# Kernel tuning notes

Hardware: AMD Instinct MI355X
Metric: run time of the kernel (lower is better)

Reference implementation:

```python
import jax, jax.numpy as jnp
import numpy as np

N_NODES = 50000
N_EDGES = 800000
D = 128
L = 3


def setup_inputs() -> dict:
    key = jax.random.key(0)
    ks = jax.random.split(key, 16)
    x = jax.random.normal(ks[0], (N_NODES, D), dtype=jnp.float32)
    edge_index = jax.random.randint(ks[1], (2, N_EDGES), 0, N_NODES, dtype=jnp.int32)
    # ensure every node has at least one incoming edge (degree > 0)
    edge_index = edge_index.at[1, :N_NODES].set(jnp.arange(N_NODES, dtype=jnp.int32))
    edge_attr = jax.random.normal(ks[2], (N_EDGES, 1), dtype=jnp.float32)
    s = 1.0 / np.sqrt(D)
    lin_w = jax.random.normal(ks[3], (L, 1, D), dtype=jnp.float32)          # edge_dim=1 -> D
    lin_b = jax.random.normal(ks[4], (L, D), dtype=jnp.float32) * s
    eps = jnp.zeros((L,), dtype=jnp.float32)                                 # initial_eps = 0, trainable
    w1 = jax.random.normal(ks[5], (L, D, D), dtype=jnp.float32) * s
    b1 = jax.random.normal(ks[6], (L, D), dtype=jnp.float32) * s
    w2 = jax.random.normal(ks[7], (L, D, D), dtype=jnp.float32) * s
    b2 = jax.random.normal(ks[8], (L, D), dtype=jnp.float32) * s
    d_cat = D + L * D
    final_w = jax.random.normal(ks[9], (d_cat, D), dtype=jnp.float32) / np.sqrt(d_cat)
    final_b = jax.random.normal(ks[10], (D,), dtype=jnp.float32) * s
    return {"x": x, "edge_index": edge_index, "edge_attr": edge_attr,
            "lin_w": lin_w, "lin_b": lin_b, "eps": eps,
            "w1": w1, "b1": b1, "w2": w2, "b2": b2,
            "final_w": final_w, "final_b": final_b}


def reference(x, edge_index, edge_attr, lin_w, lin_b, eps, w1, b1, w2, b2, final_w, final_b):
    src, tgt = edge_index[0], edge_index[1]
    n = x.shape[0]
    # degree of target nodes (float), shape [N, 1]
    deg = jax.ops.segment_sum(jnp.ones(src.shape[0], x.dtype), tgt, num_segments=n)[:, None]
    xs = [x]
    h = x
    for l in range(L):
        e = edge_attr @ lin_w[l] + lin_b[l]                  # [E, D] edge-feature projection
        msg = jax.nn.relu(h[src] + e)                        # gather + fuse + relu
        agg = jax.ops.segment_sum(msg, tgt, num_segments=n)  # scatter-add
        out = agg / deg + (1.0 + eps[l]) * h                 # degree-normalize + eps-residual
        h = jax.nn.relu(out @ w1[l] + b1[l]) @ w2[l] + b2[l] # 2-layer MLP (no BN, no dropout)
        xs.append(h)
    cat = jnp.concatenate(xs, axis=-1)                       # [N, D + L*D]
    return cat @ final_w + final_b
```

## Files before the change

kernel.cpp:

```cpp
#include <hip/hip_runtime.h>

#define NN 50000
#define NE 800000
#define DIM 128
#define NLAYERS 3

typedef __attribute__((ext_vector_type(8))) short bf16x8;
typedef __attribute__((ext_vector_type(4))) float f32x4;

__device__ __forceinline__ unsigned short f2bf_hi(float f) {
    unsigned int u = __float_as_uint(f);
    u += 0x7FFF + ((u >> 16) & 1);
    return (unsigned short)(u >> 16);
}
__device__ __forceinline__ float bf2f(unsigned short u) {
    return __uint_as_float(((unsigned int)u) << 16);
}

__global__ __launch_bounds__(256) void rank_kernel(const int* __restrict__ tgt,
                                                   int* __restrict__ counts,
                                                   int* __restrict__ rank, int E) {
    int base = (blockIdx.x * 256 + threadIdx.x) * 4;
    if (base >= E) return;
    int4 t = *(const int4*)(tgt + base);
    int4 r;
    r.x = atomicAdd(&counts[t.x], 1);
    r.y = atomicAdd(&counts[t.y], 1);
    r.z = atomicAdd(&counts[t.z], 1);
    r.w = atomicAdd(&counts[t.w], 1);
    *(int4*)(rank + base) = r;
}

__global__ __launch_bounds__(256) void scan_partial_kernel(const int* __restrict__ counts,
                                                           int* __restrict__ psum, int n) {
    __shared__ int ws[4];
    int b = blockIdx.x, t = threadIdx.x;
    int idx = b * 1024 + t * 4;
    int v = 0;
    if (idx < n) {
        int4 c = *(const int4*)(counts + idx);
        v = c.x + c.y + c.z + c.w;
    }
#pragma unroll
    for (int o = 32; o > 0; o >>= 1) v += __shfl_xor(v, o);
    int lane = t & 63, wid = t >> 6;
    if (lane == 0) ws[wid] = v;
    __syncthreads();
    if (t == 0) psum[b] = ws[0] + ws[1] + ws[2] + ws[3];
}

__global__ __launch_bounds__(64) void scan_small_kernel(const int* __restrict__ psum,
                                                        int* __restrict__ pbase,
                                                        int* __restrict__ offsets,
                                                        int nb, int n) {
    int lane = threadIdx.x;
    int v = (lane < nb) ? psum[lane] : 0;
    int incl = v;
#pragma unroll
    for (int o = 1; o < 64; o <<= 1) {
        int t = __shfl_up(incl, o);
        if (lane >= o) incl += t;
    }
    if (lane < nb) pbase[lane] = incl - v;
    if (lane == 63) offsets[n] = incl;
}

__global__ __launch_bounds__(256) void scan_apply_kernel(const int* __restrict__ counts,
                                                         const int* __restrict__ pbase,
                                                         int* __restrict__ offsets, int n) {
    __shared__ int ws[4];
    int b = blockIdx.x, t = threadIdx.x;
    int lane = t & 63, wid = t >> 6;
    int idx = b * 1024 + t * 4;
    int4 c = make_int4(0, 0, 0, 0);
    if (idx < n) c = *(const int4*)(counts + idx);
    int tsum = c.x + c.y + c.z + c.w;
    int incl = tsum;
#pragma unroll
    for (int o = 1; o < 64; o <<= 1) {
        int tt = __shfl_up(incl, o);
        if (lane >= o) incl += tt;
    }
    if (lane == 63) ws[wid] = incl;
    __syncthreads();
    int wbase = pbase[b];
    for (int w = 0; w < wid; w++) wbase += ws[w];
    if (idx < n) {
        int e0 = wbase + incl - tsum;
        int4 o;
        o.x = e0;
        o.y = e0 + c.x;
        o.z = o.y + c.y;
        o.w = o.z + c.z;
        *(int4*)(offsets + idx) = o;
    }
}

__global__ __launch_bounds__(256) void scatter2_kernel(
    const int* __restrict__ src, const int* __restrict__ tgt,
    const float* __restrict__ ea, const int* __restrict__ rank,
    const int* __restrict__ offsets, int2* __restrict__ sedge, int E) {
    int base = (blockIdx.x * 256 + threadIdx.x) * 4;
    if (base >= E) return;
    int4 s = *(const int4*)(src + base);
    int4 t = *(const int4*)(tgt + base);
    int4 r = *(const int4*)(rank + base);
    float4 a = *(const float4*)(ea + base);
    sedge[offsets[t.x] + r.x] = make_int2(s.x << 8, __float_as_int(a.x));
    sedge[offsets[t.y] + r.y] = make_int2(s.y << 8, __float_as_int(a.y));
    sedge[offsets[t.z] + r.z] = make_int2(s.z << 8, __float_as_int(a.z));
    sedge[offsets[t.w] + r.w] = make_int2(s.w << 8, __float_as_int(a.w));
}

__device__ __forceinline__ int packidx(int k, int c) {
    return (((k >> 5) << 3) + (c >> 4)) * 512 + (((k >> 3) & 3) << 7) + ((c & 15) << 3) + (k & 7);
}

#define XCVT_T 1600000

__global__ __launch_bounds__(256) void prep_kernel(
    const float* __restrict__ x, unsigned short* __restrict__ xb,
    const float* __restrict__ w1, const float* __restrict__ w2, const float* __restrict__ fw,
    unsigned short* __restrict__ w1t_h, unsigned short* __restrict__ w1t_l,
    unsigned short* __restrict__ w2t_h, unsigned short* __restrict__ w2t_l,
    unsigned short* __restrict__ fwt_h, unsigned short* __restrict__ fwt_l) {
    int gid = blockIdx.x * 256 + threadIdx.x;
    if (gid < XCVT_T) {
        int i = gid * 4;
        float4 v = *(const float4*)(x + i);
        ushort4 o;
        o.x = f2bf_hi(v.x); o.y = f2bf_hi(v.y);
        o.z = f2bf_hi(v.z); o.w = f2bf_hi(v.w);
        *(ushort4*)(xb + i) = o;
        return;
    }
    int g0 = gid - XCVT_T;
    float v; int oidx;
    unsigned short *oh, *ol;
    if (g0 < 49152) {
        int l = g0 >> 14, rem = g0 & 16383, k = rem >> 7, c = rem & 127;
        v = w1[g0]; oidx = l * 16384 + packidx(k, c); oh = w1t_h; ol = w1t_l;
    } else if (g0 < 98304) {
        int g = g0 - 49152;
        int l = g >> 14, rem = g & 16383, k = rem >> 7, c = rem & 127;
        v = w2[g]; oidx = l * 16384 + packidx(k, c); oh = w2t_h; ol = w2t_l;
    } else if (g0 < 163840) {
        int g = g0 - 98304;
        int k = g >> 7, c = g & 127;
        v = fw[g]; oidx = packidx(k, c); oh = fwt_h; ol = fwt_l;
    } else return;
    unsigned short h = f2bf_hi(v);
    float lo = v - bf2f(h);
    oh[oidx] = h;
    ol[oidx] = f2bf_hi(lo);
}

__global__ __launch_bounds__(256, 8) void agg_kernel(
    const unsigned short* __restrict__ hprev, const int* __restrict__ offs,
    const int2* __restrict__ sedge,
    const float* __restrict__ lw, const float* __restrict__ lb,
    const float* __restrict__ epsp, int layer,
    unsigned short* __restrict__ aggh, unsigned short* __restrict__ aggl, int N) {
    int g = threadIdx.x >> 4;
    int r = threadIdx.x & 15;
    int node = blockIdx.x * 16 + g;
    if (node >= N) return;
    int d0 = r * 8;
    float lwv[8], lbv[8];
    *(float4*)&lwv[0] = *(const float4*)(lw + d0);
    *(float4*)&lwv[4] = *(const float4*)(lw + d0 + 4);
    *(float4*)&lbv[0] = *(const float4*)(lb + d0);
    *(float4*)&lbv[4] = *(const float4*)(lb + d0 + 4);
    const char* hb = (const char*)hprev + r * 16;

    int s0 = offs[node], s1 = offs[node + 1];
    int sm = s1 - 1;
    int cnt = s1 - s0;
    float a[8];
#pragma unroll
    for (int c = 0; c < 8; c++) a[c] = 0.f;

    int2 e0 = sedge[s0];
    int2 e1 = sedge[min(s0 + 1, sm)];
    int2 e2 = sedge[min(s0 + 2, sm)];
    int2 e3 = sedge[min(s0 + 3, sm)];
    uint4 h0 = *(const uint4*)(hb + (unsigned)e0.x);
    uint4 h1 = *(const uint4*)(hb + (unsigned)e1.x);
    uint4 h2 = *(const uint4*)(hb + (unsigned)e2.x);

    for (int it = s0; it < s1; ++it) {
        uint4 h3 = *(const uint4*)(hb + (unsigned)e3.x);
        int2 e4 = sedge[min(it + 4, sm)];
        float wgt = __int_as_float(e0.y);
        unsigned uu[4] = {h0.x, h0.y, h0.z, h0.w};
#pragma unroll
        for (int c = 0; c < 4; c++) {
            float f0 = __uint_as_float(uu[c] << 16);
            float f1 = __uint_as_float(uu[c] & 0xffff0000u);
            a[2 * c]     += fmaxf(f0 + fmaf(wgt, lwv[2 * c], lbv[2 * c]), 0.f);
            a[2 * c + 1] += fmaxf(f1 + fmaf(wgt, lwv[2 * c + 1], lbv[2 * c + 1]), 0.f);
        }
        e0 = e1; e1 = e2; e2 = e3; e3 = e4;
        h0 = h1; h1 = h2; h2 = h3;
    }

    float inv = 1.f / (float)cnt;
    float ge = 1.f + epsp[layer];
    uint4 hs = *(const uint4*)(hb + ((unsigned)node << 8));
    unsigned su[4] = {hs.x, hs.y, hs.z, hs.w};
    unsigned short hh[8], hl[8];
#pragma unroll
    for (int c = 0; c < 4; c++) {
        float f0 = __uint_as_float(su[c] << 16);
        float f1 = __uint_as_float(su[c] & 0xffff0000u);
        float v0 = a[2 * c] * inv + ge * f0;
        float v1 = a[2 * c + 1] * inv + ge * f1;
        unsigned short h0v = f2bf_hi(v0), h1v = f2bf_hi(v1);
        hh[2 * c] = h0v; hh[2 * c + 1] = h1v;
        hl[2 * c] = f2bf_hi(v0 - bf2f(h0v));
        hl[2 * c + 1] = f2bf_hi(v1 - bf2f(h1v));
    }
    unsigned short* ph = aggh + (size_t)node * DIM + d0;
    unsigned short* pl = aggl + (size_t)node * DIM + d0;
    *(ushort4*)ph       = *(const ushort4*)&hh[0];
    *(ushort4*)(ph + 4) = *(const ushort4*)&hh[4];
    *(ushort4*)pl       = *(const ushort4*)&hl[0];
    *(ushort4*)(pl + 4) = *(const ushort4*)&hl[4];
}

#define HSTR 136

#define MLP1_LOAD(T, Bh_, Bl_, Ah_, Al_) do {                               \
    int k0_ = (T) * 32;                                                     \
    _Pragma("unroll")                                                       \
    for (int j_ = 0; j_ < 2; j_++) {                                        \
        size_t ro_ = (size_t)rowc[j_] * DIM + k0_ + q * 8;                  \
        Bh_[j_] = *(const bf16x8*)(ah_g + ro_);                             \
        Bl_[j_] = *(const bf16x8*)(al_g + ro_);                             \
    }                                                                       \
    _Pragma("unroll")                                                       \
    for (int i_ = 0; i_ < 4; i_++) {                                        \
        size_t co_ = ((size_t)((T) * 8 + wr * 4 + i_) << 9) + lane * 8;     \
        Ah_[i_] = *(const bf16x8*)(w1h + co_);                              \
        Al_[i_] = *(const bf16x8*)(w1l + co_);                              \
    }                                                                       \
} while (0)

#define MLP2_LOADW(T, Ah_, Al_) do {                                        \
    _Pragma("unroll")                                                       \
    for (int i_ = 0; i_ < 4; i_++) {                                        \
        size_t co_ = ((size_t)((T) * 8 + wr * 4 + i_) << 9) + lane * 8;     \
        Ah_[i_] = *(const bf16x8*)(w2h + co_);                              \
        Al_[i_] = *(const bf16x8*)(w2l + co_);                              \
    }                                                                       \
} while (0)

#define MLP2_LOADB(T, Bh_, Bl_) do {                                        \
    int k0_ = (T) * 32;                                                     \
    _Pragma("unroll")                                                       \
    for (int j_ = 0; j_ < 2; j_++) {                                        \
        int so_ = (wc * 32 + j_ * 16 + lr) * HSTR + k0_ + q * 8;            \
        Bh_[j_] = *(const bf16x8*)&s_hh[so_];                               \
        Bl_[j_] = *(const bf16x8*)&s_hl[so_];                               \
    }                                                                       \
} while (0)

#define MLP_MFMA(Bh_, Bl_, Ah_, Al_) do {                                   \
    _Pragma("unroll")                                                       \
    for (int i_ = 0; i_ < 4; i_++)                                          \
        _Pragma("unroll")                                                   \
        for (int j_ = 0; j_ < 2; j_++) {                                    \
            acc[i_][j_] = __builtin_amdgcn_mfma_f32_16x16x32_bf16(Ah_[i_], Bh_[j_], acc[i_][j_], 0, 0, 0); \
            acc[i_][j_] = __builtin_amdgcn_mfma_f32_16x16x32_bf16(Ah_[i_], Bl_[j_], acc[i_][j_], 0, 0, 0); \
            acc[i_][j_] = __builtin_amdgcn_mfma_f32_16x16x32_bf16(Al_[i_], Bh_[j_], acc[i_][j_], 0, 0, 0); \
        }                                                                   \
} while (0)

#define MLP_PHASES_12()                                                     \
    f32x4 acc[4][2];                                                        \
    _Pragma("unroll")                                                       \
    for (int i = 0; i < 4; i++)                                             \
        _Pragma("unroll")                                                   \
        for (int j = 0; j < 2; j++) acc[i][j] = (f32x4)(0.f);               \
    bf16x8 pBh[2], pBl[2], pAh[4], pAl[4];                                  \
    bf16x8 qBh[2], qBl[2], qAh[4], qAl[4];                                  \
    MLP1_LOAD(0, pBh, pBl, pAh, pAl);                                       \
    MLP1_LOAD(1, qBh, qBl, qAh, qAl);                                       \
    MLP_MFMA(pBh, pBl, pAh, pAl);                                           \
    MLP1_LOAD(2, pBh, pBl, pAh, pAl);                                       \
    MLP_MFMA(qBh, qBl, qAh, qAl);                                           \
    MLP1_LOAD(3, qBh, qBl, qAh, qAl);                                       \
    MLP_MFMA(pBh, pBl, pAh, pAl);                                           \
    MLP_MFMA(qBh, qBl, qAh, qAl);                                           \
    MLP2_LOADW(0, pAh, pAl);                                                \
    _Pragma("unroll")                                                       \
    for (int i = 0; i < 4; i++) {                                           \
        int hc0 = wr * 64 + i * 16 + q * 4;                                 \
        float4 bv = *(const float4*)(b1 + hc0);                             \
        float bvr[4] = {bv.x, bv.y, bv.z, bv.w};                            \
        _Pragma("unroll")                                                   \
        for (int j = 0; j < 2; j++) {                                       \
            int nl = wc * 32 + j * 16 + lr;                                 \
            unsigned short hh[4], hl[4];                                    \
            _Pragma("unroll")                                               \
            for (int r = 0; r < 4; r++) {                                   \
                float v = fmaxf(acc[i][j][r] + bvr[r], 0.f);                \
                unsigned short h = f2bf_hi(v);                              \
                hh[r] = h;                                                  \
                hl[r] = f2bf_hi(v - bf2f(h));                               \
            }                                                               \
            *(ushort4*)&s_hh[nl * HSTR + hc0] = *(const ushort4*)&hh[0];    \
            *(ushort4*)&s_hl[nl * HSTR + hc0] = *(const ushort4*)&hl[0];    \
        }                                                                   \
    }                                                                       \
    __syncthreads();                                                        \
    _Pragma("unroll")                                                       \
    for (int i = 0; i < 4; i++)                                             \
        _Pragma("unroll")                                                   \
        for (int j = 0; j < 2; j++) acc[i][j] = (f32x4)(0.f);               \
    MLP2_LOADB(0, pBh, pBl);                                                \
    MLP2_LOADW(1, qAh, qAl);                                                \
    MLP2_LOADB(1, qBh, qBl);                                                \
    MLP_MFMA(pBh, pBl, pAh, pAl);                                           \
    MLP2_LOADW(2, pAh, pAl);                                                \
    MLP2_LOADB(2, pBh, pBl);                                                \
    MLP_MFMA(qBh, qBl, qAh, qAl);                                           \
    MLP2_LOADW(3, qAh, qAl);                                                \
    MLP2_LOADB(3, qBh, qBl);                                                \
    MLP_MFMA(pBh, pBl, pAh, pAl);                                           \
    MLP_MFMA(qBh, qBl, qAh, qAl);

__global__ __launch_bounds__(256, 3) void mlp_fused(
    const unsigned short* __restrict__ ah_g, const unsigned short* __restrict__ al_g,
    const unsigned short* __restrict__ w1h, const unsigned short* __restrict__ w1l,
    const float* __restrict__ b1,
    const unsigned short* __restrict__ w2h, const unsigned short* __restrict__ w2l,
    const float* __restrict__ b2,
    unsigned short* __restrict__ out, int N) {
    __shared__ unsigned short s_hh[64 * HSTR], s_hl[64 * HSTR];
    int tid = threadIdx.x;
    int lane = tid & 63, w = tid >> 6;
    int q = lane >> 4, lr = lane & 15;
    int wr = w >> 1, wc = w & 1;
    int n0 = blockIdx.x * 64;
    int nb0 = n0 + wc * 32 + lr;
    int rowc[2];
    rowc[0] = min(nb0, N - 1);
    rowc[1] = min(nb0 + 16, N - 1);

    MLP_PHASES_12();

#pragma unroll
    for (int i = 0; i < 4; i++) {
        int hc0 = wr * 64 + i * 16 + q * 4;
        float4 bv = *(const float4*)(b2 + hc0);
        float bvr[4] = {bv.x, bv.y, bv.z, bv.w};
#pragma unroll
        for (int j = 0; j < 2; j++) {
            int node = nb0 + j * 16;
            if (node < N) {
                unsigned short o[4];
#pragma unroll
                for (int r = 0; r < 4; r++) o[r] = f2bf_hi(acc[i][j][r] + bvr[r]);
                *(ushort4*)&out[(size_t)node * DIM + hc0] = *(const ushort4*)&o[0];
            }
        }
    }
}

#define FIN3_LOADG(T, Bv_, Ah_, Al_) do {                                   \
    const unsigned short* asrc_ = srcs3[(T) >> 2];                          \
    int kk_ = ((T) & 3) * 32;                                               \
    _Pragma("unroll")                                                       \
    for (int j_ = 0; j_ < 2; j_++) {                                        \
        size_t ro_ = (size_t)rowc[j_] * DIM + kk_ + q * 8;                  \
        Bv_[j_] = *(const bf16x8*)(asrc_ + ro_);                            \
    }                                                                       \
    _Pragma("unroll")                                                       \
    for (int i_ = 0; i_ < 4; i_++) {                                        \
        size_t co_ = ((size_t)((T) * 8 + wr * 4 + i_) << 9) + lane * 8;     \
        Ah_[i_] = *(const bf16x8*)(fwh + co_);                              \
        Al_[i_] = *(const bf16x8*)(fwl + co_);                              \
    }                                                                       \
} while (0)

#define FIN_MFMA(Bv_, Ah_, Al_) do {                                        \
    _Pragma("unroll")                                                       \
    for (int i_ = 0; i_ < 4; i_++)                                          \
        _Pragma("unroll")                                                   \
        for (int j_ = 0; j_ < 2; j_++) {                                    \
            acc[i_][j_] = __builtin_amdgcn_mfma_f32_16x16x32_bf16(Ah_[i_], Bv_[j_], acc[i_][j_], 0, 0, 0); \
            acc[i_][j_] = __builtin_amdgcn_mfma_f32_16x16x32_bf16(Al_[i_], Bv_[j_], acc[i_][j_], 0, 0, 0); \
        }                                                                   \
} while (0)

#define FIN3_STEPL(T) do {                                                  \
    int kk_ = ((T) - 12) * 32;                                              \
    bf16x8 Bh_[2], Bl_[2], Ah_[4], Al_[4];                                  \
    _Pragma("unroll")                                                       \
    for (int j_ = 0; j_ < 2; j_++) {                                        \
        int so_ = (wc * 32 + j_ * 16 + lr) * HSTR + kk_ + q * 8;            \
        Bh_[j_] = *(const bf16x8*)&s_hh[so_];                               \
        Bl_[j_] = *(const bf16x8*)&s_hl[so_];                               \
    }                                                                       \
    _Pragma("unroll")                                                       \
    for (int i_ = 0; i_ < 4; i_++) {                                        \
        size_t co_ = ((size_t)((T) * 8 + wr * 4 + i_) << 9) + lane * 8;     \
        Ah_[i_] = *(const bf16x8*)(fwh + co_);                              \
        Al_[i_] = *(const bf16x8*)(fwl + co_);                              \
    }                                                                       \
    _Pragma("unroll")                                                       \
    for (int i_ = 0; i_ < 4; i_++)                                          \
        _Pragma("unroll")                                                   \
        for (int j_ = 0; j_ < 2; j_++) {                                    \
            acc[i_][j_] = __builtin_amdgcn_mfma_f32_16x16x32_bf16(Ah_[i_], Bh_[j_], acc[i_][j_], 0, 0, 0); \
            acc[i_][j_] = __builtin_amdgcn_mfma_f32_16x16x32_bf16(Ah_[i_], Bl_[j_], acc[i_][j_], 0, 0, 0); \
            acc[i_][j_] = __builtin_amdgcn_mfma_f32_16x16x32_bf16(Al_[i_], Bh_[j_], acc[i_][j_], 0, 0, 0); \
        }                                                                   \
} while (0)

__global__ __launch_bounds__(256, 3) void mlp_final_fused(
    const unsigned short* __restrict__ ah_g, const unsigned short* __restrict__ al_g,
    const unsigned short* __restrict__ w1h, const unsigned short* __restrict__ w1l,
    const float* __restrict__ b1,
    const unsigned short* __restrict__ w2h, const unsigned short* __restrict__ w2l,
    const float* __restrict__ b2,
    const unsigned short* __restrict__ xsrc, const unsigned short* __restrict__ h0p,
    const unsigned short* __restrict__ h1p,
    const unsigned short* __restrict__ fwh, const unsigned short* __restrict__ fwl,
    const float* __restrict__ fbias, float* __restrict__ out, int N) {
    __shared__ unsigned short s_hh[64 * HSTR], s_hl[64 * HSTR];
    int tid = threadIdx.x;
    int lane = tid & 63, w = tid >> 6;
    int q = lane >> 4, lr = lane & 15;
    int wr = w >> 1, wc = w & 1;
    int n0 = blockIdx.x * 64;
    int nb0 = n0 + wc * 32 + lr;
    int rowc[2];
    rowc[0] = min(nb0, N - 1);
    rowc[1] = min(nb0 + 16, N - 1);

    MLP_PHASES_12();

    __syncthreads();

#pragma unroll
    for (int i = 0; i < 4; i++) {
        int hc0 = wr * 64 + i * 16 + q * 4;
        float4 bv = *(const float4*)(b2 + hc0);
        float bvr[4] = {bv.x, bv.y, bv.z, bv.w};
#pragma unroll
        for (int j = 0; j < 2; j++) {
            int nl = wc * 32 + j * 16 + lr;
            unsigned short hh[4], hl[4];
#pragma unroll
            for (int r = 0; r < 4; r++) {
                float v = acc[i][j][r] + bvr[r];
                unsigned short h = f2bf_hi(v);
                hh[r] = h;
                hl[r] = f2bf_hi(v - bf2f(h));
            }
            *(ushort4*)&s_hh[nl * HSTR + hc0] = *(const ushort4*)&hh[0];
            *(ushort4*)&s_hl[nl * HSTR + hc0] = *(const ushort4*)&hl[0];
        }
    }

#pragma unroll
    for (int i = 0; i < 4; i++)
#pragma unroll
        for (int j = 0; j < 2; j++) acc[i][j] = (f32x4)(0.f);

    const unsigned short* srcs3[3] = {xsrc, h0p, h1p};
    bf16x8 pB[2], pWh[4], pWl[4];
    bf16x8 qB[2], qWh[4], qWl[4];
    FIN3_LOADG(0, pB, pWh, pWl);
    FIN3_LOADG(1, qB, qWh, qWl);
    __syncthreads();

#pragma unroll
    for (int t = 0; t < 12; t += 2) {
        FIN_MFMA(pB, pWh, pWl);
        if (t + 2 < 12) FIN3_LOADG(t + 2, pB, pWh, pWl);
        FIN_MFMA(qB, qWh, qWl);
        if (t + 3 < 12) FIN3_LOADG(t + 3, qB, qWh, qWl);
    }
    FIN3_STEPL(12);
    FIN3_STEPL(13);
    FIN3_STEPL(14);
    FIN3_STEPL(15);

#pragma unroll
    for (int i = 0; i < 4; i++) {
        int hc0 = wr * 64 + i * 16 + q * 4;
        float4 bv = *(const float4*)(fbias + hc0);
        float bvr[4] = {bv.x, bv.y, bv.z, bv.w};
#pragma unroll
        for (int j = 0; j < 2; j++) {
            int node = nb0 + j * 16;
            if (node < N) {
                float4 o;
                o.x = acc[i][j][0] + bvr[0];
                o.y = acc[i][j][1] + bvr[1];
                o.z = acc[i][j][2] + bvr[2];
                o.w = acc[i][j][3] + bvr[3];
                *(float4*)&out[(size_t)node * DIM + hc0] = o;
            }
        }
    }
}

extern "C" void kernel_launch(void* const* d_in, const int* in_sizes, int n_in,
                              void* d_out, int out_size, void* d_ws, size_t ws_size,
                              hipStream_t stream) {
    const float* x   = (const float*)d_in[0];
    const int* edge_index = (const int*)d_in[1];
    const float* ea  = (const float*)d_in[2];
    const float* lw  = (const float*)d_in[3];
    const float* lb  = (const float*)d_in[4];
    const float* eps = (const float*)d_in[5];
    const float* w1  = (const float*)d_in[6];
    const float* b1  = (const float*)d_in[7];
    const float* w2  = (const float*)d_in[8];
    const float* b2  = (const float*)d_in[9];
    const float* fw  = (const float*)d_in[10];
    const float* fb  = (const float*)d_in[11];
    float* out = (float*)d_out;

    const int N = NN, E = NE;
    const int* src = edge_index;
    const int* tgt = edge_index + E;
    const int NB = (N + 1023) / 1024;

    char* ws = (char*)d_ws;
    size_t off = 0;
    auto alloc = [&](size_t bytes) {
        void* p = ws + off;
        off += (bytes + 255) & ~(size_t)255;
        return p;
    };
    int*   counts  = (int*)alloc((size_t)N * 4);
    int*   offsets = (int*)alloc((size_t)(N + 1) * 4);
    int*   rank    = (int*)alloc((size_t)E * 4);
    int*   psum    = (int*)alloc((size_t)NB * 4);
    int*   pbase   = (int*)alloc((size_t)NB * 4);
    int2*  sedge   = (int2*)alloc((size_t)E * 8);
    unsigned short* w1t_h = (unsigned short*)alloc(49152 * 2);
    unsigned short* w1t_l = (unsigned short*)alloc(49152 * 2);
    unsigned short* w2t_h = (unsigned short*)alloc(49152 * 2);
    unsigned short* w2t_l = (unsigned short*)alloc(49152 * 2);
    unsigned short* fwt_h = (unsigned short*)alloc(65536 * 2);
    unsigned short* fwt_l = (unsigned short*)alloc(65536 * 2);
    unsigned short* xb    = (unsigned short*)alloc((size_t)N * DIM * 2);
    unsigned short* hbuf[2];
    for (int i = 0; i < 2; i++) hbuf[i] = (unsigned short*)alloc((size_t)N * DIM * 2);
    unsigned short* aggh = (unsigned short*)alloc((size_t)N * DIM * 2);
    unsigned short* aggl = (unsigned short*)alloc((size_t)N * DIM * 2);
    (void)ws_size; (void)in_sizes; (void)n_in; (void)out_size;

    hipMemsetAsync(counts, 0, (size_t)N * 4, stream);
    rank_kernel<<<(E / 4 + 255) / 256, 256, 0, stream>>>(tgt, counts, rank, E);
    prep_kernel<<<(XCVT_T + 163840 + 255) / 256, 256, 0, stream>>>(
        x, xb, w1, w2, fw, w1t_h, w1t_l, w2t_h, w2t_l, fwt_h, fwt_l);
    scan_partial_kernel<<<NB, 256, 0, stream>>>(counts, psum, N);
    scan_small_kernel<<<1, 64, 0, stream>>>(psum, pbase, offsets, NB, N);
    scan_apply_kernel<<<NB, 256, 0, stream>>>(counts, pbase, offsets, N);
    scatter2_kernel<<<(E / 4 + 255) / 256, 256, 0, stream>>>(src, tgt, ea, rank, offsets, sedge, E);

    const int GB = (N + 63) / 64;
    const int AB = (N + 15) / 16;
    for (int l = 0; l < 2; l++) {
        const unsigned short* hin = (l == 0) ? xb : hbuf[l - 1];
        agg_kernel<<<AB, 256, 0, stream>>>(hin, offsets, sedge,
            lw + l * DIM, lb + l * DIM, eps, l, aggh, aggl, N);
        mlp_fused<<<GB, 256, 0, stream>>>(
            aggh, aggl,
            w1t_h + l * 16384, w1t_l + l * 16384, b1 + l * DIM,
            w2t_h + l * 16384, w2t_l + l * 16384, b2 + l * DIM,
            hbuf[l], N);
    }
    agg_kernel<<<AB, 256, 0, stream>>>(hbuf[1], offsets, sedge,
        lw + 2 * DIM, lb + 2 * DIM, eps, 2, aggh, aggl, N);
    mlp_final_fused<<<GB, 256, 0, stream>>>(
        aggh, aggl,
        w1t_h + 2 * 16384, w1t_l + 2 * 16384, b1 + 2 * DIM,
        w2t_h + 2 * 16384, w2t_l + 2 * 16384, b2 + 2 * DIM,
        xb, hbuf[0], hbuf[1], fwt_h, fwt_l, fb, out, N);
}
```

Baseline: 354.2 us.

## Degree-sort nodes for aggregation and fuse scans into one-block kernel

Replaces the three-kernel prefix scan with a single 256-thread block that computes CSR offsets and also counting-sorts nodes by in-degree into a permutation. The aggregation kernel then walks nodes in degree order so each block's 16 node groups have similar edge counts, reducing load imbalance between neighbouring nodes. The counts memset is folded into the prep kernel, and prep now runs before the rank kernel. Risks: the single-block scan is serial over 50k entries and may take longer than the old multi-block scan, and permuted node order scatters the agg output writes.

```diff
diff --git a/kernel.cpp b/kernel.cpp
--- a/kernel.cpp
+++ b/kernel.cpp
@@ -31,68 +31,68 @@
     *(int4*)(rank + base) = r;
 }
 
-__global__ __launch_bounds__(256) void scan_partial_kernel(const int* __restrict__ counts,
-                                                           int* __restrict__ psum, int n) {
+__global__ __launch_bounds__(256) void scan_sort_kernel(const int* __restrict__ counts,
+                                                        int* __restrict__ offsets,
+                                                        int* __restrict__ perm, int n) {
     __shared__ int ws[4];
-    int b = blockIdx.x, t = threadIdx.x;
-    int idx = b * 1024 + t * 4;
-    int v = 0;
-    if (idx < n) {
-        int4 c = *(const int4*)(counts + idx);
-        v = c.x + c.y + c.z + c.w;
-    }
-#pragma unroll
-    for (int o = 32; o > 0; o >>= 1) v += __shfl_xor(v, o);
+    __shared__ int bins[64];
+    __shared__ int binbase[64];
+    const int C = 196;
+    int t = threadIdx.x;
+    if (t < 64) bins[t] = 0;
+    __syncthreads();
+    int beg = t * C;
+    int end = min(beg + C, n);
+    int s = 0;
+    for (int i = beg; i < end; i += 4) {
+        int4 c4 = *(const int4*)(counts + i);
+        s += c4.x + c4.y + c4.z + c4.w;
+        atomicAdd(&bins[min(c4.x, 63)], 1);
+        atomicAdd(&bins[min(c4.y, 63)], 1);
+        atomicAdd(&bins[min(c4.z, 63)], 1);
+        atomicAdd(&bins[min(c4.w, 63)], 1);
+    }
     int lane = t & 63, wid = t >> 6;
-    if (lane == 0) ws[wid] = v;
-    __syncthreads();
-    if (t == 0) psum[b] = ws[0] + ws[1] + ws[2] + ws[3];
-}
-
-__global__ __launch_bounds__(64) void scan_small_kernel(const int* __restrict__ psum,
-                                                        int* __restrict__ pbase,
-                                                        int* __restrict__ offsets,
-                                                        int nb, int n) {
-    int lane = threadIdx.x;
-    int v = (lane < nb) ? psum[lane] : 0;
-    int incl = v;
+    int incl = s;
 #pragma unroll
     for (int o = 1; o < 64; o <<= 1) {
-        int t = __shfl_up(incl, o);
-        if (lane >= o) incl += t;
-    }
-    if (lane < nb) pbase[lane] = incl - v;
-    if (lane == 63) offsets[n] = incl;
-}
-
-__global__ __launch_bounds__(256) void scan_apply_kernel(const int* __restrict__ counts,
-                                                         const int* __restrict__ pbase,
-                                                         int* __restrict__ offsets, int n) {
-    __shared__ int ws[4];
-    int b = blockIdx.x, t = threadIdx.x;
-    int lane = t & 63, wid = t >> 6;
-    int idx = b * 1024 + t * 4;
-    int4 c = make_int4(0, 0, 0, 0);
-    if (idx < n) c = *(const int4*)(counts + idx);
-    int tsum = c.x + c.y + c.z + c.w;
-    int incl = tsum;
-#pragma unroll
-    for (int o = 1; o < 64; o <<= 1) {
-        int tt = __shfl_up(incl, o);
-        if (lane >= o) incl += tt;
+        int u = __shfl_up(incl, o);
+        if (lane >= o) incl += u;
     }
     if (lane == 63) ws[wid] = incl;
     __syncthreads();
-    int wbase = pbase[b];
+    int wbase = 0;
     for (int w = 0; w < wid; w++) wbase += ws[w];
-    if (idx < n) {
-        int e0 = wbase + incl - tsum;
-        int4 o;
-        o.x = e0;
-        o.y = e0 + c.x;
-        o.z = o.y + c.y;
-        o.w = o.z + c.z;
-        *(int4*)(offsets + idx) = o;
+    int run = wbase + incl - s;
+    for (int i = beg; i < end; i += 4) {
+        int4 c4 = *(const int4*)(counts + i);
+        int4 o4;
+        o4.x = run;
+        o4.y = run + c4.x;
+        o4.z = o4.y + c4.y;
+        o4.w = o4.z + c4.z;
+        run = o4.w + c4.w;
+        *(int4*)(offsets + i) = o4;
+    }
+    if (t == 255) offsets[n] = run;
+    __syncthreads();
+    if (t < 64) {
+        int v = bins[t];
+        int bincl = v;
+#pragma unroll
+        for (int o = 1; o < 64; o <<= 1) {
+            int u = __shfl_up(bincl, o);
+            if (t >= o) bincl += u;
+        }
+        binbase[t] = bincl - v;
+    }
+    __syncthreads();
+    if (t < 64) bins[t] = binbase[t];
+    __syncthreads();
+    for (int i = beg; i < end; ++i) {
+        int d = min(counts[i], 63);
+        int pos = atomicAdd(&bins[d], 1);
+        perm[pos] = i;
     }
 }
 
@@ -116,17 +116,24 @@
     return (((k >> 5) << 3) + (c >> 4)) * 512 + (((k >> 3) & 3) << 7) + ((c & 15) << 3) + (k & 7);
 }
 
+#define ZERO_T 12500
 #define XCVT_T 1600000
 
 __global__ __launch_bounds__(256) void prep_kernel(
+    int* __restrict__ counts,
     const float* __restrict__ x, unsigned short* __restrict__ xb,
     const float* __restrict__ w1, const float* __restrict__ w2, const float* __restrict__ fw,
     unsigned short* __restrict__ w1t_h, unsigned short* __restrict__ w1t_l,
     unsigned short* __restrict__ w2t_h, unsigned short* __restrict__ w2t_l,
     unsigned short* __restrict__ fwt_h, unsigned short* __restrict__ fwt_l) {
     int gid = blockIdx.x * 256 + threadIdx.x;
-    if (gid < XCVT_T) {
-        int i = gid * 4;
+    if (gid < ZERO_T) {
+        *(int4*)(counts + gid * 4) = make_int4(0, 0, 0, 0);
+        return;
+    }
+    int g1 = gid - ZERO_T;
+    if (g1 < XCVT_T) {
+        int i = g1 * 4;
         float4 v = *(const float4*)(x + i);
         ushort4 o;
         o.x = f2bf_hi(v.x); o.y = f2bf_hi(v.y);
@@ -134,7 +141,7 @@
         *(ushort4*)(xb + i) = o;
         return;
     }
-    int g0 = gid - XCVT_T;
+    int g0 = g1 - XCVT_T;
     float v; int oidx;
     unsigned short *oh, *ol;
     if (g0 < 49152) {
@@ -157,14 +164,15 @@
 
 __global__ __launch_bounds__(256, 8) void agg_kernel(
     const unsigned short* __restrict__ hprev, const int* __restrict__ offs,
-    const int2* __restrict__ sedge,
+    const int2* __restrict__ sedge, const int* __restrict__ perm,
     const float* __restrict__ lw, const float* __restrict__ lb,
     const float* __restrict__ epsp, int layer,
     unsigned short* __restrict__ aggh, unsigned short* __restrict__ aggl, int N) {
     int g = threadIdx.x >> 4;
     int r = threadIdx.x & 15;
-    int node = blockIdx.x * 16 + g;
-    if (node >= N) return;
+    int idx = blockIdx.x * 16 + g;
+    if (idx >= N) return;
+    int node = perm[idx];
     int d0 = r * 8;
     float lwv[8], lbv[8];
     *(float4*)&lwv[0] = *(const float4*)(lw + d0);
@@ -529,7 +537,6 @@
     const int N = NN, E = NE;
     const int* src = edge_index;
     const int* tgt = edge_index + E;
-    const int NB = (N + 1023) / 1024;
 
     char* ws = (char*)d_ws;
     size_t off = 0;
@@ -540,9 +547,8 @@
     };
     int*   counts  = (int*)alloc((size_t)N * 4);
     int*   offsets = (int*)alloc((size_t)(N + 1) * 4);
+    int*   perm    = (int*)alloc((size_t)N * 4);
     int*   rank    = (int*)alloc((size_t)E * 4);
-    int*   psum    = (int*)alloc((size_t)NB * 4);
-    int*   pbase   = (int*)alloc((size_t)NB * 4);
     int2*  sedge   = (int2*)alloc((size_t)E * 8);
     unsigned short* w1t_h = (unsigned short*)alloc(49152 * 2);
     unsigned short* w1t_l = (unsigned short*)alloc(49152 * 2);
@@ -557,20 +563,18 @@
     unsigned short* aggl = (unsigned short*)alloc((size_t)N * DIM * 2);
     (void)ws_size; (void)in_sizes; (void)n_in; (void)out_size;
 
-    hipMemsetAsync(counts, 0, (size_t)N * 4, stream);
+    const int PREP_T = ZERO_T + XCVT_T + 163840;
+    prep_kernel<<<(PREP_T + 255) / 256, 256, 0, stream>>>(
+        counts, x, xb, w1, w2, fw, w1t_h, w1t_l, w2t_h, w2t_l, fwt_h, fwt_l);
     rank_kernel<<<(E / 4 + 255) / 256, 256, 0, stream>>>(tgt, counts, rank, E);
-    prep_kernel<<<(XCVT_T + 163840 + 255) / 256, 256, 0, stream>>>(
-        x, xb, w1, w2, fw, w1t_h, w1t_l, w2t_h, w2t_l, fwt_h, fwt_l);
-    scan_partial_kernel<<<NB, 256, 0, stream>>>(counts, psum, N);
-    scan_small_kernel<<<1, 64, 0, stream>>>(psum, pbase, offsets, NB, N);
-    scan_apply_kernel<<<NB, 256, 0, stream>>>(counts, pbase, offsets, N);
+    scan_sort_kernel<<<1, 256, 0, stream>>>(counts, offsets, perm, N);
     scatter2_kernel<<<(E / 4 + 255) / 256, 256, 0, stream>>>(src, tgt, ea, rank, offsets, sedge, E);
 
     const int GB = (N + 63) / 64;
     const int AB = (N + 15) / 16;
     for (int l = 0; l < 2; l++) {
         const unsigned short* hin = (l == 0) ? xb : hbuf[l - 1];
-        agg_kernel<<<AB, 256, 0, stream>>>(hin, offsets, sedge,
+        agg_kernel<<<AB, 256, 0, stream>>>(hin, offsets, sedge, perm,
             lw + l * DIM, lb + l * DIM, eps, l, aggh, aggl, N);
         mlp_fused<<<GB, 256, 0, stream>>>(
             aggh, aggl,
@@ -578,7 +582,7 @@
             w2t_h + l * 16384, w2t_l + l * 16384, b2 + l * DIM,
             hbuf[l], N);
     }
-    agg_kernel<<<AB, 256, 0, stream>>>(hbuf[1], offsets, sedge,
+    agg_kernel<<<AB, 256, 0, stream>>>(hbuf[1], offsets, sedge, perm,
         lw + 2 * DIM, lb + 2 * DIM, eps, 2, aggh, aggl, N);
     mlp_final_fused<<<GB, 256, 0, stream>>>(
         aggh, aggl,
```

Result: slower. 429.4 us (+21.2%).
